# Kernel optimization log

Hardware: AMD Instinct MI355X
Metric: run time of the kernel (lower is better)

Reference implementation:

```python
import jax, jax.numpy as jnp
import numpy as np

LATENT = 292
T = 120          # max_length
CHARSET = 35     # charset_length
B = 512
H1, H2, H3 = 701, 701, 901


def _p(key, shape, scale=0.05):
    return jax.random.normal(key, shape, dtype=jnp.float32) * scale


def setup_inputs() -> dict:
    key = jax.random.key(0)
    ks = jax.random.split(key, 12)
    z32 = lambda *s: jnp.zeros(s, jnp.float32)
    return {
        "z": jax.random.normal(ks[0], (B, LATENT), dtype=jnp.float32),
        # linear_1: Dense(latent_dim, selu)
        "W1": _p(ks[1], (LATENT, LATENT)), "b1": z32(LATENT),
        # gru_1 (Keras GRU, reset_after=True): kernel [in,3H], recurrent [H,3H], two bias vectors [3H]
        "gWi1": _p(ks[2], (LATENT, 3 * H1)), "gWh1": _p(ks[3], (H1, 3 * H1)),
        "gbi1": z32(3 * H1), "gbh1": z32(3 * H1),
        # gru_2
        "gWi2": _p(ks[4], (H1, 3 * H2)), "gWh2": _p(ks[5], (H2, 3 * H2)),
        "gbi2": z32(3 * H2), "gbh2": z32(3 * H2),
        # gru_3
        "gWi3": _p(ks[6], (H2, 3 * H3)), "gWh3": _p(ks[7], (H3, 3 * H3)),
        "gbi3": z32(3 * H3), "gbh3": z32(3 * H3),
        # linear_2: TimeDistributed(Dense(charset_length))
        "Wo": _p(ks[8], (H3, CHARSET)), "bo": z32(CHARSET),
    }


def _gru(x_seq, Wi, Wh, bi, bh):
    """Keras GRU (reset_after=True, gate order z,r,h), return_sequences=True.
    x_seq: [B,T,D] -> [B,T,H]. Input projections hoisted out of the scan."""
    H = Wh.shape[0]
    bsz = x_seq.shape[0]
    xp = jnp.einsum('btd,dg->btg', x_seq, Wi) + bi  # [B,T,3H]
    xp = jnp.transpose(xp, (1, 0, 2))               # [T,B,3H] for scan
    h0 = jnp.zeros((bsz, H), x_seq.dtype)

    def step(h, xt):
        rp = h @ Wh + bh                             # recurrent projection [B,3H]
        xz, xr, xh = jnp.split(xt, 3, axis=-1)
        rz, rr, rh = jnp.split(rp, 3, axis=-1)
        zg = jax.nn.sigmoid(xz + rz)
        rg = jax.nn.sigmoid(xr + rr)
        hh = jnp.tanh(xh + rg * rh)                  # reset applied after recurrent matmul
        hn = zg * h + (1.0 - zg) * hh
        return hn, hn

    _, ys = jax.lax.scan(step, h0, xp)               # ys: [T,B,H]
    return jnp.transpose(ys, (1, 0, 2))


def reference(z, W1, b1, gWi1, gWh1, gbi1, gbh1, gWi2, gWh2, gbi2, gbh2,
              gWi3, gWh3, gbi3, gbh3, Wo, bo):
    x = jax.nn.selu(z @ W1 + b1)                             # [B,latent]
    xs = jnp.broadcast_to(x[:, None, :], (x.shape[0], T, x.shape[1]))  # RepeatVector
    h = _gru(xs, gWi1, gWh1, gbi1, gbh1)                     # [B,T,701]
    h = _gru(h, gWi2, gWh2, gbi2, gbh2)                      # [B,T,701] (dropout inactive at inference)
    h = _gru(h, gWi3, gWh3, gbi3, gbh3)                      # [B,T,901]
    logits = jnp.einsum('bth,hc->btc', h, Wo) + bo           # [B,T,charset]
    return jax.nn.softmax(logits, axis=2)
```

## Files before the change

### kernel.cpp

```cpp
#include <hip/hip_runtime.h>
#include <hip/hip_bf16.h>
#include <math.h>

typedef unsigned short u16;
typedef __attribute__((ext_vector_type(4))) float f32x4;
typedef __attribute__((ext_vector_type(8))) short s16x8;

#define BB  512
#define TT  120
#define LAT 292
#define HH1 701
#define HH3 901
#define H1P 704
#define H3P 960
#define CH  35

static const size_t O_X    = 0;
static const size_t O_XP1  = 598016;
static const size_t O_H1F  = 4923392;
static const size_t O_H2F  = 7806976;
static const size_t O_H3F  = 10690560;
static const size_t O_H1B  = 14622720;
static const size_t O_H2B  = 16064512;
static const size_t O_H3B  = 17506304;
static const size_t O_WHT1 = 19472384;
static const size_t O_WIT2 = 22446080;
static const size_t O_WHT2 = 25419776;
static const size_t O_WIT3 = 28393472;
static const size_t O_WHT3 = 32358400;
static const size_t O_WOT  = 37765120;
static const size_t O_TAB  = 37888000;
static const size_t ZERO_BYTES = 14548992;

#define DSWZ(row, g) ((((g) ^ ((row) & 7)) << 4))

static __device__ __forceinline__ u16 f2b(float f){
  union { float f; unsigned int i; } v; v.f = f;
  unsigned int x = v.i;
  return (u16)((x + 0x7FFFu + ((x >> 16) & 1u)) >> 16);
}

#define GLL16(g, l) __builtin_amdgcn_global_load_lds( \
    (const __attribute__((address_space(1))) unsigned int*)(g), \
    (__attribute__((address_space(3))) unsigned int*)(l), 16, 0, 0)

__launch_bounds__(256)
__global__ void k_selu(const float* __restrict__ z, const float* __restrict__ W1,
                       const float* __restrict__ b1, float* __restrict__ x)
{
  int idx = blockIdx.x * 256 + threadIdx.x;
  if (idx >= BB * LAT) return;
  int b = idx / LAT, i = idx - b * LAT;
  float acc = b1[i];
  const float* zr = z + (size_t)b * LAT;
  for (int k = 0; k < LAT; ++k)
    acc += zr[k] * W1[k * LAT + i];
  const float alpha = 1.6732632423543772f, scale = 1.0507009873554805f;
  x[idx] = scale * (acc > 0.f ? acc : alpha * (expf(acc) - 1.f));
}

__launch_bounds__(256)
__global__ void k_xp1(const float* __restrict__ x, const float* __restrict__ Wi1,
                      const float* __restrict__ bi1, float* __restrict__ xp1)
{
  int nb = blockIdx.x % 9, bb = blockIdx.x / 9;
  int n = nb * 256 + threadIdx.x;
  int b0 = bb * 8;
  if (n >= 2112) return;
  if (n >= 2103) { for (int r = 0; r < 8; ++r) xp1[(size_t)(b0 + r) * 2112 + n] = 0.f; return; }
  float bias = bi1[n];
  float acc[8];
  for (int r = 0; r < 8; ++r) acc[r] = bias;
  for (int k = 0; k < LAT; ++k) {
    float w = Wi1[(size_t)k * 2103 + n];
    #pragma unroll
    for (int r = 0; r < 8; ++r) acc[r] += x[(size_t)(b0 + r) * LAT + k] * w;
  }
  for (int r = 0; r < 8; ++r) xp1[(size_t)(b0 + r) * 2112 + n] = acc[r];
}

__launch_bounds__(256)
__global__ void k_transpose(const float* __restrict__ W, u16* __restrict__ WT,
                            int K, int N, int Kpad, int RowsPad)
{
  int tilesN = RowsPad / 64;
  int tk = blockIdx.x / tilesN, tn = blockIdx.x % tilesN;
  int k0 = tk * 64, n0 = tn * 64;
  __shared__ u16 lds[64][72];
  int tid = threadIdx.x;
  int nl = tid & 63, q = tid >> 6;
  for (int i = 0; i < 16; ++i) {
    int kl = q * 16 + i;
    int k = k0 + kl, n = n0 + nl;
    lds[kl][nl] = (k < K && n < N) ? f2b(W[(size_t)k * N + n]) : (u16)0;
  }
  __syncthreads();
  for (int i = 0; i < 16; ++i) {
    int rl = q * 16 + i;
    WT[(size_t)(n0 + rl) * Kpad + k0 + nl] = lds[nl][rl];
  }
}

__global__ void k_maketab(unsigned int* __restrict__ tab)
{
  if (threadIdx.x != 0 || blockIdx.x != 0) return;
  for (int x = 0; x < 8; ++x) {
    for (int li = 0; li < 32; ++li) {
      unsigned v;
      if (li < 15) {
        int t3 = 15 * x + li;
        v = 0xFFFF0000u | (2u << 12) | ((unsigned)(t3 & 7) << 8) | (unsigned)(t3 >> 3);
      } else if (li < 26) {
        int t2 = 11 * x + (li - 15);
        v = 0xFFFF0000u | (1u << 12) | ((unsigned)(t2 & 7) << 8) | (unsigned)(t2 >> 3);
      } else if (li < 31) {
        int pi = 5 * x + (li - 26);
        int i0 = 2 * pi, i1 = 2 * pi + 1;
        unsigned lo = ((unsigned)(i0 & 7) << 8) | (unsigned)(i0 >> 3);
        unsigned hw = ((unsigned)(i1 & 7) << 8) | (unsigned)(i1 >> 3);
        v = lo | (hw << 16);
      } else {
        if (x < 4) {
          unsigned lo = (3u << 12) | ((unsigned)(2 * x) << 8);
          unsigned hw = (3u << 12) | ((unsigned)(2 * x + 1) << 8);
          v = lo | (hw << 16);
        } else {
          int pi = 40 + (x - 4);
          int i0 = 2 * pi, i1 = 2 * pi + 1;
          unsigned lo = ((unsigned)(i0 & 7) << 8) | (unsigned)(i0 >> 3);
          unsigned hw = ((unsigned)(i1 & 7) << 8) | (unsigned)(i1 >> 3);
          v = lo | (hw << 16);
        }
      }
      tab[x + 8 * li] = v;
    }
  }
}


static __device__ __forceinline__ void stage_gru(
    const u16* __restrict__ A, int As, const u16* __restrict__ W, int Ws, int WH,
    int r0, int j0, int kbase, int wl, int lane, char* buf)
{
  #pragma unroll
  for (int i = 0; i < 8; ++i) {
    int slot = wl * 512 + i * 64 + lane;
    const u16* g;
    if (slot < 512) {
      int row = slot >> 3, gl = slot & 7;
      int gq = gl ^ (row & 7);
      g = A + (size_t)(r0 + row) * As + kbase + gq * 8;
    } else {
      int s2 = slot - 512;
      int gate = s2 >> 9, loc = s2 & 511;
      int col = loc >> 3, gl = loc & 7;
      int gq = gl ^ (col & 7);
      g = W + ((size_t)gate * WH + j0 + col) * Ws + kbase + gq * 8;
    }
    char* l = buf + (wl * 512 + i * 64) * 16;
    GLL16(g, l);
  }
}

template<int HACC>
static __device__ __forceinline__ void mm_gru(const char* gb, int wr, int wc, int m16, int kg,
                                              f32x4 (&acc)[4][2][2])
{
  #pragma unroll
  for (int s = 0; s < 2; ++s) {
    s16x8 af[2];
    #pragma unroll
    for (int fm = 0; fm < 2; ++fm) {
      int row = wr * 32 + fm * 16 + m16;
      af[fm] = *(const s16x8*)(gb + row * 128 + DSWZ(row, s * 4 + kg));
    }
    #pragma unroll
    for (int g = 0; g < 3; ++g) {
      #pragma unroll
      for (int fn = 0; fn < 2; ++fn) {
        int col = wc * 32 + fn * 16 + m16;
        s16x8 bf = *(const s16x8*)(gb + 8192 + g * 8192 + col * 128 + DSWZ(col, s * 4 + kg));
        const int ai = (g == 2) ? HACC : g;
        #pragma unroll
        for (int fm = 0; fm < 2; ++fm)
          acc[ai][fm][fn] = __builtin_amdgcn_mfma_f32_16x16x32_bf16(af[fm], bf, acc[ai][fm][fn], 0, 0, 0);
      }
    }
  }
}

static __device__ __forceinline__ void gru_pipe(
    const u16* A0, int As0, const u16* W0, int Ws0,
    const u16* A1, int As1, const u16* W1p, int Ws1,
    int WH, int n0, int n1, int k1off,
    int r0, int j0, char* g0, char* g1, int wl, int lane,
    int wr, int wc, int m16, int kg, f32x4 (&acc)[4][2][2])
{
  const int n = n0 + n1;
#define STG(C, BUF) do { int c_ = (C); \
    if (c_ < n0) stage_gru(A0, As0, W0, Ws0, WH, r0, j0, c_ * 64, wl, lane, (BUF)); \
    else         stage_gru(A1, As1, W1p, Ws1, WH, r0, j0, (c_ - n0) * 64 + k1off, wl, lane, (BUF)); \
  } while (0)
  STG(0, g0);
  __syncthreads();
  for (int ch = 0; ch < n; ch += 2) {
    if (ch + 1 < n) STG(ch + 1, g1);
    if (ch < n0) mm_gru<2>(g0, wr, wc, m16, kg, acc);
    else         mm_gru<3>(g0, wr, wc, m16, kg, acc);
    __syncthreads();
    if (ch + 1 >= n) break;
    if (ch + 2 < n) STG(ch + 2, g0);
    if (ch + 1 < n0) mm_gru<2>(g1, wr, wc, m16, kg, acc);
    else             mm_gru<3>(g1, wr, wc, m16, kg, acc);
    __syncthreads();
  }
#undef STG
}

__launch_bounds__(512, 2)
__global__ void k_wave(int s, const unsigned int* __restrict__ tab,
    const u16* __restrict__ WhT1, const u16* __restrict__ WiT2, const u16* __restrict__ WhT2,
    const u16* __restrict__ WiT3, const u16* __restrict__ WhT3, const u16* __restrict__ WoT,
    const float* __restrict__ xp1,
    const float* __restrict__ gbh1,
    const float* __restrict__ gbi2, const float* __restrict__ gbh2,
    const float* __restrict__ gbi3, const float* __restrict__ gbh3,
    const float* __restrict__ bo,
    float* __restrict__ h1f, u16* __restrict__ h1b,
    float* __restrict__ h2f, u16* __restrict__ h2b,
    float* __restrict__ h3f, u16* __restrict__ h3b,
    float* __restrict__ out)
{
  extern __shared__ __align__(16) char smem[];
  const int tid  = threadIdx.x;
  const int wgrp = tid >> 8;
  const int ltid = tid & 255;
  const int lane = tid & 63;
  const int wl   = (tid >> 6) & 3;
  const int wr = wl >> 1, wc = wl & 1;
  const int m16 = lane & 15, kg = lane >> 4;
  char* g0 = smem + wgrp * 65536;
  char* g1 = g0 + 32768;

  const unsigned e  = tab[blockIdx.x];
  const unsigned lo = e & 0xFFFFu, hi = e >> 16;
  const bool ksplit = (hi == 0xFFFFu);
  const unsigned item = (!ksplit && wgrp == 1) ? hi : lo;
  const int L  = (item >> 12) & 3;
  const int rr = (item >> 8) & 0xF;
  const int cc = item & 0xFF;
  const int t = s - L;
  if (t < 0 || t >= TT) return;
  const int cur = s & 1, prv = cur ^ 1;

  if (L == 3) {
    const int r0 = rr * 64;
    const u16* Ab = h3b + (size_t)prv * BB * H3P;
    f32x4 acc2[2][2];
    { f32x4 z4 = {0.f,0.f,0.f,0.f}; for (int a=0;a<2;++a) for (int b=0;b<2;++b) acc2[a][b]=z4; }
    int4 ra[2], rb2[2];
    const int n = H3P / 64;
    #pragma unroll
    for (int it = 0; it < 2; ++it) {
      int gi = it * 256 + ltid; int r = gi >> 3, gq = gi & 7;
      ra[it]  = *(const int4*)(Ab + (size_t)(r0 + r) * H3P + gq * 8);
      rb2[it] = *(const int4*)(WoT + (size_t)r * H3P + gq * 8);
    }
    #pragma unroll
    for (int it = 0; it < 2; ++it) {
      int gi = it * 256 + ltid; int r = gi >> 3, gq = gi & 7;
      *(int4*)(g0 + r * 128 + DSWZ(r, gq)) = ra[it];
      *(int4*)(g0 + 8192 + r * 128 + DSWZ(r, gq)) = rb2[it];
    }
    __syncthreads();
    for (int ch = 0; ch < n; ++ch) {
      const bool have = (ch + 1 < n);
      if (have) {
        int kb = (ch + 1) * 64;
        #pragma unroll
        for (int it = 0; it < 2; ++it) {
          int gi = it * 256 + ltid; int r = gi >> 3, gq = gi & 7;
          ra[it]  = *(const int4*)(Ab + (size_t)(r0 + r) * H3P + kb + gq * 8);
          rb2[it] = *(const int4*)(WoT + (size_t)r * H3P + kb + gq * 8);
        }
      }
      #pragma unroll
      for (int s2 = 0; s2 < 2; ++s2) {
        s16x8 af[2], bf[2];
        #pragma unroll
        for (int fm = 0; fm < 2; ++fm) {
          int row = wr * 32 + fm * 16 + m16;
          af[fm] = *(const s16x8*)(g0 + row * 128 + DSWZ(row, s2 * 4 + kg));
        }
        #pragma unroll
        for (int fn = 0; fn < 2; ++fn) {
          int col = wc * 32 + fn * 16 + m16;
          bf[fn] = *(const s16x8*)(g0 + 8192 + col * 128 + DSWZ(col, s2 * 4 + kg));
        }
        #pragma unroll
        for (int fm = 0; fm < 2; ++fm)
          #pragma unroll
          for (int fn = 0; fn < 2; ++fn)
            acc2[fm][fn] = __builtin_amdgcn_mfma_f32_16x16x32_bf16(af[fm], bf[fn], acc2[fm][fn], 0, 0, 0);
      }
      if (have) {
        __syncthreads();
        #pragma unroll
        for (int it = 0; it < 2; ++it) {
          int gi = it * 256 + ltid; int r = gi >> 3, gq = gi & 7;
          *(int4*)(g0 + r * 128 + DSWZ(r, gq)) = ra[it];
          *(int4*)(g0 + 8192 + r * 128 + DSWZ(r, gq)) = rb2[it];
        }
        __syncthreads();
      }
    }
    __syncthreads();
    float (*ldsL)[68] = (float (*)[68])g0;
    #pragma unroll
    for (int fn = 0; fn < 2; ++fn) {
      int col = wc * 32 + fn * 16 + m16;
      float bov = (col < CH) ? bo[col] : 0.f;
      #pragma unroll
      for (int fm = 0; fm < 2; ++fm)
        #pragma unroll
        for (int ii = 0; ii < 4; ++ii)
          ldsL[wr * 32 + fm * 16 + kg * 4 + ii][col] = acc2[fm][fn][ii] + bov;
    }
    __syncthreads();
    if (ltid < 64) {
      int b = r0 + ltid;
      float mx = -1e30f;
      for (int c2 = 0; c2 < CH; ++c2) mx = fmaxf(mx, ldsL[ltid][c2]);
      float sum = 0.f;
      for (int c2 = 0; c2 < CH; ++c2) sum += expf(ldsL[ltid][c2] - mx);
      float inv = 1.f / sum;
      size_t ob = ((size_t)b * TT + t) * CH;
      for (int c2 = 0; c2 < CH; ++c2) out[ob + c2] = expf(ldsL[ltid][c2] - mx) * inv;
    }
    return;
  }

  int H, HP;
  const u16 *A0 = nullptr, *W0 = nullptr, *A1 = nullptr, *W1p = nullptr;
  int As0 = 0, Ws0 = 0, As1 = 0, Ws1 = 0, n0 = 0, n1 = 0, k1off = 0;
  const float *bi = nullptr, *bh;
  float *hfP, *hfC; u16 *hbC;
  if (L == 0) {
    H = HH1; HP = H1P;
    A1 = h1b + (size_t)prv * BB * H1P; As1 = H1P; W1p = WhT1; Ws1 = H1P; n1 = 11;
    bh = gbh1;
    hfP = h1f + (size_t)prv * BB * H1P; hfC = h1f + (size_t)cur * BB * H1P;
    hbC = h1b + (size_t)cur * BB * H1P;
  } else if (L == 1) {
    H = HH1; HP = H1P;
    bi = gbi2; bh = gbh2;
    hfP = h2f + (size_t)prv * BB * H1P; hfC = h2f + (size_t)cur * BB * H1P;
    hbC = h2b + (size_t)cur * BB * H1P;
    if (wgrp == 0) { A0 = h1b + (size_t)prv * BB * H1P; As0 = H1P; W0 = WiT2; Ws0 = H1P; n0 = 11; }
    else           { A1 = h2b + (size_t)prv * BB * H1P; As1 = H1P; W1p = WhT2; Ws1 = H1P; n1 = 11; }
  } else {
    H = HH3; HP = H3P;
    bi = gbi3; bh = gbh3;
    hfP = h3f + (size_t)prv * BB * H3P; hfC = h3f + (size_t)cur * BB * H3P;
    hbC = h3b + (size_t)cur * BB * H3P;
    if (wgrp == 0) {
      A0 = h2b + (size_t)prv * BB * H1P; As0 = H1P; W0 = WiT3; Ws0 = H1P; n0 = 11;
      A1 = h3b + (size_t)prv * BB * H3P; As1 = H3P; W1p = WhT3; Ws1 = H3P; n1 = 2; k1off = 0;
    } else {
      A1 = h3b + (size_t)prv * BB * H3P; As1 = H3P; W1p = WhT3; Ws1 = H3P; n1 = 13; k1off = 128;
    }
  }
  const int r0 = rr * 64, j0 = cc * 64;

  f32x4 acc[4][2][2];
  {
    f32x4 z4 = {0.f, 0.f, 0.f, 0.f};
    for (int g = 0; g < 4; ++g) for (int a = 0; a < 2; ++a) for (int b = 0; b < 2; ++b) acc[g][a][b] = z4;
  }

  gru_pipe(A0, As0, W0, Ws0, A1, As1, W1p, Ws1, H, n0, n1, k1off,
           r0, j0, g0, g1, wl, lane, wr, wc, m16, kg, acc);

  if (ksplit) {
    __syncthreads();
    float* red = (float*)smem;
    if (wgrp == 1) {
      float* b = red + ltid * 64;
      #pragma unroll
      for (int g = 0; g < 4; ++g)
        #pragma unroll
        for (int fm = 0; fm < 2; ++fm)
          #pragma unroll
          for (int fn = 0; fn < 2; ++fn)
            *(f32x4*)(b + ((g * 2 + fm) * 2 + fn) * 4) = acc[g][fm][fn];
    }
    __syncthreads();
    if (wgrp == 1) return;
    {
      const float* b = red + ltid * 64;
      #pragma unroll
      for (int g = 0; g < 4; ++g)
        #pragma unroll
        for (int fm = 0; fm < 2; ++fm)
          #pragma unroll
          for (int fn = 0; fn < 2; ++fn)
            acc[g][fm][fn] += *(const f32x4*)(b + ((g * 2 + fm) * 2 + fn) * 4);
    }
  }

  #pragma unroll
  for (int fn = 0; fn < 2; ++fn) {
    int j = j0 + wc * 32 + fn * 16 + m16;
    if (j >= H) continue;
    float bhz = bh[j], bhr = bh[H + j], bhh = bh[2 * H + j];
    float biz = 0.f, bir = 0.f, bih = 0.f;
    if (L != 0) { biz = bi[j]; bir = bi[H + j]; bih = bi[2 * H + j]; }
    #pragma unroll
    for (int fm = 0; fm < 2; ++fm) {
      #pragma unroll
      for (int ii = 0; ii < 4; ++ii) {
        int row = r0 + wr * 32 + fm * 16 + kg * 4 + ii;
        float az  = acc[0][fm][fn][ii];
        float ar  = acc[1][fm][fn][ii];
        float axh = acc[2][fm][fn][ii];
        float arh = acc[3][fm][fn][ii];
        float pz, pr, xh_, rh_;
        if (L == 0) {
          const float* xr_ = xp1 + (size_t)row * 2112;
          pz  = xr_[j] + az + bhz;
          pr  = xr_[HH1 + j] + ar + bhr;
          xh_ = xr_[2 * HH1 + j];
          rh_ = arh + bhh;
        } else {
          pz  = az + biz + bhz;
          pr  = ar + bir + bhr;
          xh_ = axh + bih;
          rh_ = arh + bhh;
        }
        float zg = 1.f / (1.f + expf(-pz));
        float rg = 1.f / (1.f + expf(-pr));
        float hh = tanhf(xh_ + rg * rh_);
        float hp = hfP[(size_t)row * HP + j];
        float hn = zg * hp + (1.f - zg) * hh;
        hfC[(size_t)row * HP + j] = hn;
        hbC[(size_t)row * HP + j] = f2b(hn);
      }
    }
  }
}

extern "C" void kernel_launch(void* const* d_in, const int* in_sizes, int n_in,
                              void* d_out, int out_size, void* d_ws, size_t ws_size,
                              hipStream_t stream)
{
  const float* z    = (const float*)d_in[0];
  const float* W1   = (const float*)d_in[1];
  const float* b1   = (const float*)d_in[2];
  const float* gWi1 = (const float*)d_in[3];
  const float* gWh1 = (const float*)d_in[4];
  const float* gbi1 = (const float*)d_in[5];
  const float* gbh1 = (const float*)d_in[6];
  const float* gWi2 = (const float*)d_in[7];
  const float* gWh2 = (const float*)d_in[8];
  const float* gbi2 = (const float*)d_in[9];
  const float* gbh2 = (const float*)d_in[10];
  const float* gWi3 = (const float*)d_in[11];
  const float* gWh3 = (const float*)d_in[12];
  const float* gbi3 = (const float*)d_in[13];
  const float* gbh3 = (const float*)d_in[14];
  const float* Wo   = (const float*)d_in[15];
  const float* bo   = (const float*)d_in[16];

  char* ws = (char*)d_ws;
  float* x_f  = (float*)(ws + O_X);
  float* xp1  = (float*)(ws + O_XP1);
  float* h1f  = (float*)(ws + O_H1F);
  float* h2f  = (float*)(ws + O_H2F);
  float* h3f  = (float*)(ws + O_H3F);
  u16*   h1b  = (u16*)(ws + O_H1B);
  u16*   h2b  = (u16*)(ws + O_H2B);
  u16*   h3b  = (u16*)(ws + O_H3B);
  u16*   WhT1 = (u16*)(ws + O_WHT1);
  u16*   WiT2 = (u16*)(ws + O_WIT2);
  u16*   WhT2 = (u16*)(ws + O_WHT2);
  u16*   WiT3 = (u16*)(ws + O_WIT3);
  u16*   WhT3 = (u16*)(ws + O_WHT3);
  u16*   WoT  = (u16*)(ws + O_WOT);
  unsigned int* tab = (unsigned int*)(ws + O_TAB);

  hipFuncSetAttribute((const void*)k_wave,
                      hipFuncAttributeMaxDynamicSharedMemorySize, 131072);

  hipMemsetAsync(ws + O_H1F, 0, ZERO_BYTES, stream);

  k_maketab<<<1, 64, 0, stream>>>(tab);
  k_selu<<<(BB * LAT + 255) / 256, 256, 0, stream>>>(z, W1, b1, x_f);
  k_xp1<<<9 * 64, 256, 0, stream>>>(x_f, gWi1, gbi1, xp1);

  k_transpose<<<11 * 33, 256, 0, stream>>>(gWh1, WhT1, 701, 2103, 704, 2112);
  k_transpose<<<11 * 33, 256, 0, stream>>>(gWi2, WiT2, 701, 2103, 704, 2112);
  k_transpose<<<11 * 33, 256, 0, stream>>>(gWh2, WhT2, 701, 2103, 704, 2112);
  k_transpose<<<11 * 44, 256, 0, stream>>>(gWi3, WiT3, 701, 2703, 704, 2816);
  k_transpose<<<15 * 44, 256, 0, stream>>>(gWh3, WhT3, 901, 2703, 960, 2816);
  k_transpose<<<15 * 1, 256, 0, stream>>>(Wo, WoT, 901, 35, 960, 64);

  for (int s = 0; s < TT + 3; ++s)
    k_wave<<<256, 512, 131072, stream>>>(s, tab, WhT1, WiT2, WhT2, WiT3, WhT3, WoT, xp1,
                                         gbh1, gbi2, gbh2, gbi3, gbh3, bo,
                                         h1f, h1b, h2f, h2b, h3f, h3b, (float*)d_out);
}
```

Baseline: 4.983 ms.

## Group wave work items by layer per XCD and cache x in LDS

Rebuilds the block-to-work table so each XCD (blockIdx mod 8) gets contiguous runs of tiles from the same layer. Previously every XCD got an interleaved mix of layer-1, layer-2, layer-3 and output tiles. The goal is that each XCD's L2 only holds one or two layers' transposed weights, which should improve weight reuse in L2. The risk is uneven load across XCDs, since layer-3 k-split tiles are heavier than the others. It also stages x rows in LDS in the one-time xp1 kernel and moves the output/softmax tile into a helper function.

```diff
diff --git a/kernel.cpp b/kernel.cpp
--- a/kernel.cpp
+++ b/kernel.cpp
@@ -14,6 +14,7 @@
 #define H1P 704
 #define H3P 960
 #define CH  35
+#define NSTEP (TT + 3)
 
 static const size_t O_X    = 0;
 static const size_t O_XP1  = 598016;
@@ -30,7 +31,7 @@
 static const size_t O_WHT3 = 32358400;
 static const size_t O_WOT  = 37765120;
 static const size_t O_TAB  = 37888000;
-static const size_t ZERO_BYTES = 14548992;
+static const size_t ZERO_SMALL = 14548992;
 
 #define DSWZ(row, g) ((((g) ^ ((row) & 7)) << 4))
 
@@ -63,9 +64,13 @@
 __global__ void k_xp1(const float* __restrict__ x, const float* __restrict__ Wi1,
                       const float* __restrict__ bi1, float* __restrict__ xp1)
 {
+  __shared__ float xs[8][LAT];
   int nb = blockIdx.x % 9, bb = blockIdx.x / 9;
   int n = nb * 256 + threadIdx.x;
   int b0 = bb * 8;
+  for (int i = threadIdx.x; i < 8 * LAT; i += 256)
+    xs[i / LAT][i % LAT] = x[(size_t)(b0 + i / LAT) * LAT + (i % LAT)];
+  __syncthreads();
   if (n >= 2112) return;
   if (n >= 2103) { for (int r = 0; r < 8; ++r) xp1[(size_t)(b0 + r) * 2112 + n] = 0.f; return; }
   float bias = bi1[n];
@@ -74,7 +79,7 @@
   for (int k = 0; k < LAT; ++k) {
     float w = Wi1[(size_t)k * 2103 + n];
     #pragma unroll
-    for (int r = 0; r < 8; ++r) acc[r] += x[(size_t)(b0 + r) * LAT + k] * w;
+    for (int r = 0; r < 8; ++r) acc[r] += xs[r][k] * w;
   }
   for (int r = 0; r < 8; ++r) xp1[(size_t)(b0 + r) * 2112 + n] = acc[r];
 }
@@ -104,39 +109,37 @@
 __global__ void k_maketab(unsigned int* __restrict__ tab)
 {
   if (threadIdx.x != 0 || blockIdx.x != 0) return;
+  int g3 = 0, g2 = 0, g1p = 0, outp = 0;
   for (int x = 0; x < 8; ++x) {
     for (int li = 0; li < 32; ++li) {
+      int kind;
+      if (x <= 2)      kind = 0;
+      else if (x == 3) kind = (li < 24) ? 0 : 1;
+      else if (x <= 5) kind = 1;
+      else if (x == 6) kind = (li < 16) ? 1 : 2;
+      else             kind = (li < 28) ? 2 : 3;
       unsigned v;
-      if (li < 15) {
-        int t3 = 15 * x + li;
+      if (kind == 0) {
+        int t3 = g3++;
         v = 0xFFFF0000u | (2u << 12) | ((unsigned)(t3 & 7) << 8) | (unsigned)(t3 >> 3);
-      } else if (li < 26) {
-        int t2 = 11 * x + (li - 15);
+      } else if (kind == 1) {
+        int t2 = g2++;
         v = 0xFFFF0000u | (1u << 12) | ((unsigned)(t2 & 7) << 8) | (unsigned)(t2 >> 3);
-      } else if (li < 31) {
-        int pi = 5 * x + (li - 26);
-        int i0 = 2 * pi, i1 = 2 * pi + 1;
+      } else if (kind == 2) {
+        int i0 = 2 * g1p, i1 = 2 * g1p + 1; g1p++;
         unsigned lo = ((unsigned)(i0 & 7) << 8) | (unsigned)(i0 >> 3);
         unsigned hw = ((unsigned)(i1 & 7) << 8) | (unsigned)(i1 >> 3);
         v = lo | (hw << 16);
       } else {
-        if (x < 4) {
-          unsigned lo = (3u << 12) | ((unsigned)(2 * x) << 8);
-          unsigned hw = (3u << 12) | ((unsigned)(2 * x + 1) << 8);
-          v = lo | (hw << 16);
-        } else {
-          int pi = 40 + (x - 4);
-          int i0 = 2 * pi, i1 = 2 * pi + 1;
-          unsigned lo = ((unsigned)(i0 & 7) << 8) | (unsigned)(i0 >> 3);
-          unsigned hw = ((unsigned)(i1 & 7) << 8) | (unsigned)(i1 >> 3);
-          v = lo | (hw << 16);
-        }
+        unsigned lo = (3u << 12) | ((unsigned)(2 * outp) << 8);
+        unsigned hw = (3u << 12) | ((unsigned)(2 * outp + 1) << 8);
+        outp++;
+        v = lo | (hw << 16);
       }
       tab[x + 8 * li] = v;
     }
   }
 }
-
 
 static __device__ __forceinline__ void stage_gru(
     const u16* __restrict__ A, int As, const u16* __restrict__ W, int Ws, int WH,
@@ -217,8 +220,96 @@
 #undef STG
 }
 
+static __device__ __forceinline__ void out_tile(
+    const u16* __restrict__ Ab, const u16* __restrict__ WoT, const float* __restrict__ bo,
+    float* __restrict__ out, int r0, int t,
+    char* g0, int ltid, int wr, int wc, int m16, int kg)
+{
+  f32x4 acc2[2][2];
+  { f32x4 z4 = {0.f,0.f,0.f,0.f}; for (int a=0;a<2;++a) for (int b=0;b<2;++b) acc2[a][b]=z4; }
+  int4 ra[2], rb2[2];
+  const int n = H3P / 64;
+  #pragma unroll
+  for (int it = 0; it < 2; ++it) {
+    int gi = it * 256 + ltid; int r = gi >> 3, gq = gi & 7;
+    ra[it]  = *(const int4*)(Ab + (size_t)(r0 + r) * H3P + gq * 8);
+    rb2[it] = *(const int4*)(WoT + (size_t)r * H3P + gq * 8);
+  }
+  #pragma unroll
+  for (int it = 0; it < 2; ++it) {
+    int gi = it * 256 + ltid; int r = gi >> 3, gq = gi & 7;
+    *(int4*)(g0 + r * 128 + DSWZ(r, gq)) = ra[it];
+    *(int4*)(g0 + 8192 + r * 128 + DSWZ(r, gq)) = rb2[it];
+  }
+  __syncthreads();
+  for (int ch = 0; ch < n; ++ch) {
+    const bool have = (ch + 1 < n);
+    if (have) {
+      int kb = (ch + 1) * 64;
+      #pragma unroll
+      for (int it = 0; it < 2; ++it) {
+        int gi = it * 256 + ltid; int r = gi >> 3, gq = gi & 7;
+        ra[it]  = *(const int4*)(Ab + (size_t)(r0 + r) * H3P + kb + gq * 8);
+        rb2[it] = *(const int4*)(WoT + (size_t)r * H3P + kb + gq * 8);
+      }
+    }
+    #pragma unroll
+    for (int s2 = 0; s2 < 2; ++s2) {
+      s16x8 af[2], bf[2];
+      #pragma unroll
+      for (int fm = 0; fm < 2; ++fm) {
+        int row = wr * 32 + fm * 16 + m16;
+        af[fm] = *(const s16x8*)(g0 + row * 128 + DSWZ(row, s2 * 4 + kg));
+      }
+      #pragma unroll
+      for (int fn = 0; fn < 2; ++fn) {
+        int col = wc * 32 + fn * 16 + m16;
+        bf[fn] = *(const s16x8*)(g0 + 8192 + col * 128 + DSWZ(col, s2 * 4 + kg));
+      }
+      #pragma unroll
+      for (int fm = 0; fm < 2; ++fm)
+        #pragma unroll
+        for (int fn = 0; fn < 2; ++fn)
+          acc2[fm][fn] = __builtin_amdgcn_mfma_f32_16x16x32_bf16(af[fm], bf[fn], acc2[fm][fn], 0, 0, 0);
+    }
+    if (have) {
+      __syncthreads();
+      #pragma unroll
+      for (int it = 0; it < 2; ++it) {
+        int gi = it * 256 + ltid; int r = gi >> 3, gq = gi & 7;
+        *(int4*)(g0 + r * 128 + DSWZ(r, gq)) = ra[it];
+        *(int4*)(g0 + 8192 + r * 128 + DSWZ(r, gq)) = rb2[it];
+      }
+      __syncthreads();
+    }
+  }
+  __syncthreads();
+  float (*ldsL)[68] = (float (*)[68])g0;
+  #pragma unroll
+  for (int fn = 0; fn < 2; ++fn) {
+    int col = wc * 32 + fn * 16 + m16;
+    float bov = (col < CH) ? bo[col] : 0.f;
+    #pragma unroll
+    for (int fm = 0; fm < 2; ++fm)
+      #pragma unroll
+      for (int ii = 0; ii < 4; ++ii)
+        ldsL[wr * 32 + fm * 16 + kg * 4 + ii][col] = acc2[fm][fn][ii] + bov;
+  }
+  __syncthreads();
+  if (ltid < 64) {
+    int b = r0 + ltid;
+    float mx = -1e30f;
+    for (int c2 = 0; c2 < CH; ++c2) mx = fmaxf(mx, ldsL[ltid][c2]);
+    float sum = 0.f;
+    for (int c2 = 0; c2 < CH; ++c2) sum += expf(ldsL[ltid][c2] - mx);
+    float inv = 1.f / sum;
+    size_t ob = ((size_t)b * TT + t) * CH;
+    for (int c2 = 0; c2 < CH; ++c2) out[ob + c2] = expf(ldsL[ltid][c2] - mx) * inv;
+  }
+}
+
 __launch_bounds__(512, 2)
-__global__ void k_wave(int s, const unsigned int* __restrict__ tab,
+__global__ void k_wave9(int s, const unsigned int* __restrict__ tab,
     const u16* __restrict__ WhT1, const u16* __restrict__ WiT2, const u16* __restrict__ WhT2,
     const u16* __restrict__ WiT3, const u16* __restrict__ WhT3, const u16* __restrict__ WoT,
     const float* __restrict__ xp1,
@@ -254,113 +345,29 @@
   const int cur = s & 1, prv = cur ^ 1;
 
   if (L == 3) {
-    const int r0 = rr * 64;
-    const u16* Ab = h3b + (size_t)prv * BB * H3P;
-    f32x4 acc2[2][2];
-    { f32x4 z4 = {0.f,0.f,0.f,0.f}; for (int a=0;a<2;++a) for (int b=0;b<2;++b) acc2[a][b]=z4; }
-    int4 ra[2], rb2[2];
-    const int n = H3P / 64;
-    #pragma unroll
-    for (int it = 0; it < 2; ++it) {
-      int gi = it * 256 + ltid; int r = gi >> 3, gq = gi & 7;
-      ra[it]  = *(const int4*)(Ab + (size_t)(r0 + r) * H3P + gq * 8);
-      rb2[it] = *(const int4*)(WoT + (size_t)r * H3P + gq * 8);
-    }
-    #pragma unroll
-    for (int it = 0; it < 2; ++it) {
-      int gi = it * 256 + ltid; int r = gi >> 3, gq = gi & 7;
-      *(int4*)(g0 + r * 128 + DSWZ(r, gq)) = ra[it];
-      *(int4*)(g0 + 8192 + r * 128 + DSWZ(r, gq)) = rb2[it];
-    }
-    __syncthreads();
-    for (int ch = 0; ch < n; ++ch) {
-      const bool have = (ch + 1 < n);
-      if (have) {
-        int kb = (ch + 1) * 64;
-        #pragma unroll
-        for (int it = 0; it < 2; ++it) {
-          int gi = it * 256 + ltid; int r = gi >> 3, gq = gi & 7;
-          ra[it]  = *(const int4*)(Ab + (size_t)(r0 + r) * H3P + kb + gq * 8);
-          rb2[it] = *(const int4*)(WoT + (size_t)r * H3P + kb + gq * 8);
-        }
-      }
-      #pragma unroll
-      for (int s2 = 0; s2 < 2; ++s2) {
-        s16x8 af[2], bf[2];
-        #pragma unroll
-        for (int fm = 0; fm < 2; ++fm) {
-          int row = wr * 32 + fm * 16 + m16;
-          af[fm] = *(const s16x8*)(g0 + row * 128 + DSWZ(row, s2 * 4 + kg));
-        }
-        #pragma unroll
-        for (int fn = 0; fn < 2; ++fn) {
-          int col = wc * 32 + fn * 16 + m16;
-          bf[fn] = *(const s16x8*)(g0 + 8192 + col * 128 + DSWZ(col, s2 * 4 + kg));
-        }
-        #pragma unroll
-        for (int fm = 0; fm < 2; ++fm)
-          #pragma unroll
-          for (int fn = 0; fn < 2; ++fn)
-            acc2[fm][fn] = __builtin_amdgcn_mfma_f32_16x16x32_bf16(af[fm], bf[fn], acc2[fm][fn], 0, 0, 0);
-      }
-      if (have) {
-        __syncthreads();
-        #pragma unroll
-        for (int it = 0; it < 2; ++it) {
-          int gi = it * 256 + ltid; int r = gi >> 3, gq = gi & 7;
-          *(int4*)(g0 + r * 128 + DSWZ(r, gq)) = ra[it];
-          *(int4*)(g0 + 8192 + r * 128 + DSWZ(r, gq)) = rb2[it];
-        }
-        __syncthreads();
-      }
-    }
-    __syncthreads();
-    float (*ldsL)[68] = (float (*)[68])g0;
-    #pragma unroll
-    for (int fn = 0; fn < 2; ++fn) {
-      int col = wc * 32 + fn * 16 + m16;
-      float bov = (col < CH) ? bo[col] : 0.f;
-      #pragma unroll
-      for (int fm = 0; fm < 2; ++fm)
-        #pragma unroll
-        for (int ii = 0; ii < 4; ++ii)
-          ldsL[wr * 32 + fm * 16 + kg * 4 + ii][col] = acc2[fm][fn][ii] + bov;
-    }
-    __syncthreads();
-    if (ltid < 64) {
-      int b = r0 + ltid;
-      float mx = -1e30f;
-      for (int c2 = 0; c2 < CH; ++c2) mx = fmaxf(mx, ldsL[ltid][c2]);
-      float sum = 0.f;
-      for (int c2 = 0; c2 < CH; ++c2) sum += expf(ldsL[ltid][c2] - mx);
-      float inv = 1.f / sum;
-      size_t ob = ((size_t)b * TT + t) * CH;
-      for (int c2 = 0; c2 < CH; ++c2) out[ob + c2] = expf(ldsL[ltid][c2] - mx) * inv;
-    }
+    out_tile(h3b + (size_t)prv * BB * H3P, WoT, bo, out, rr * 64, t, g0, ltid, wr, wc, m16, kg);
     return;
   }
 
-  int H, HP;
+  int H;
   const u16 *A0 = nullptr, *W0 = nullptr, *A1 = nullptr, *W1p = nullptr;
   int As0 = 0, Ws0 = 0, As1 = 0, Ws1 = 0, n0 = 0, n1 = 0, k1off = 0;
   const float *bi = nullptr, *bh;
   float *hfP, *hfC; u16 *hbC;
   if (L == 0) {
-    H = HH1; HP = H1P;
+    H = HH1;
     A1 = h1b + (size_t)prv * BB * H1P; As1 = H1P; W1p = WhT1; Ws1 = H1P; n1 = 11;
     bh = gbh1;
     hfP = h1f + (size_t)prv * BB * H1P; hfC = h1f + (size_t)cur * BB * H1P;
     hbC = h1b + (size_t)cur * BB * H1P;
   } else if (L == 1) {
-    H = HH1; HP = H1P;
-    bi = gbi2; bh = gbh2;
+    H = HH1; bi = gbi2; bh = gbh2;
     hfP = h2f + (size_t)prv * BB * H1P; hfC = h2f + (size_t)cur * BB * H1P;
     hbC = h2b + (size_t)cur * BB * H1P;
-    if (wgrp == 0) { A0 = h1b + (size_t)prv * BB * H1P; As0 = H1P; W0 = WiT2; Ws0 = H1P; n0 = 11; }
+    if (wgrp == 0) { A0 = h1b + (size_t)prv * BB * H1P; As0 = H1P; W0 = WiT2; Ws0 = H1P; n0 = 11; As1 = H1P; }
     else           { A1 = h2b + (size_t)prv * BB * H1P; As1 = H1P; W1p = WhT2; Ws1 = H1P; n1 = 11; }
   } else {
-    H = HH3; HP = H3P;
-    bi = gbi3; bh = gbh3;
+    H = HH3; bi = gbi3; bh = gbh3;
     hfP = h3f + (size_t)prv * BB * H3P; hfC = h3f + (size_t)cur * BB * H3P;
     hbC = h3b + (size_t)cur * BB * H3P;
     if (wgrp == 0) {
@@ -373,10 +380,8 @@
   const int r0 = rr * 64, j0 = cc * 64;
 
   f32x4 acc[4][2][2];
-  {
-    f32x4 z4 = {0.f, 0.f, 0.f, 0.f};
-    for (int g = 0; g < 4; ++g) for (int a = 0; a < 2; ++a) for (int b = 0; b < 2; ++b) acc[g][a][b] = z4;
-  }
+  { f32x4 z4 = {0.f, 0.f, 0.f, 0.f};
+    for (int g = 0; g < 4; ++g) for (int a = 0; a < 2; ++a) for (int b = 0; b < 2; ++b) acc[g][a][b] = z4; }
 
   gru_pipe(A0, As0, W0, Ws0, A1, As1, W1p, Ws1, H, n0, n1, k1off,
            r0, j0, g0, g1, wl, lane, wr, wc, m16, kg, acc);
@@ -440,10 +445,10 @@
         float zg = 1.f / (1.f + expf(-pz));
         float rg = 1.f / (1.f + expf(-pr));
         float hh = tanhf(xh_ + rg * rh_);
-        float hp = hfP[(size_t)row * HP + j];
+        float hp = hfP[(size_t)row * As1 + j];
         float hn = zg * hp + (1.f - zg) * hh;
-        hfC[(size_t)row * HP + j] = hn;
-        hbC[(size_t)row * HP + j] = f2b(hn);
+        hfC[(size_t)row * As1 + j] = hn;
+        hbC[(size_t)row * As1 + j] = f2b(hn);
       }
     }
   }
@@ -488,10 +493,10 @@
   u16*   WoT  = (u16*)(ws + O_WOT);
   unsigned int* tab = (unsigned int*)(ws + O_TAB);
 
-  hipFuncSetAttribute((const void*)k_wave,
-                      hipFuncAttributeMaxDynamicSharedMemorySize, 131072);
-
-  hipMemsetAsync(ws + O_H1F, 0, ZERO_BYTES, stream);
+  (void)hipFuncSetAttribute((const void*)k_wave9,
+                            hipFuncAttributeMaxDynamicSharedMemorySize, 131072);
+
+  (void)hipMemsetAsync(ws + O_H1F, 0, ZERO_SMALL, stream);
 
   k_maketab<<<1, 64, 0, stream>>>(tab);
   k_selu<<<(BB * LAT + 255) / 256, 256, 0, stream>>>(z, W1, b1, x_f);
@@ -504,8 +509,9 @@
   k_transpose<<<15 * 44, 256, 0, stream>>>(gWh3, WhT3, 901, 2703, 960, 2816);
   k_transpose<<<15 * 1, 256, 0, stream>>>(Wo, WoT, 901, 35, 960, 64);
 
-  for (int s = 0; s < TT + 3; ++s)
-    k_wave<<<256, 512, 131072, stream>>>(s, tab, WhT1, WiT2, WhT2, WiT3, WhT3, WoT, xp1,
-                                         gbh1, gbi2, gbh2, gbi3, gbh3, bo,
-                                         h1f, h1b, h2f, h2b, h3f, h3b, (float*)d_out);
-}
+  for (int s = 0; s < NSTEP; ++s)
+    k_wave9<<<256, 512, 131072, stream>>>(s, tab,
+        WhT1, WiT2, WhT2, WiT3, WhT3, WoT, xp1,
+        gbh1, gbi2, gbh2, gbi3, gbh3, bo,
+        h1f, h1b, h2f, h2b, h3f, h3b, (float*)d_out);
+}
```

Measured after the change: 4.928 ms. About the same (-1.1%).
